# Kernel tuning notes

Hardware: AMD Instinct MI355X
Metric: run time of the kernel (lower is better)

The kernel has to match this reference:

```python
import jax, jax.numpy as jnp
import numpy as np

BATCH = 64
ORIGINAL_DIM = 524288
PROJ_DIM = 8192
C = 4


def setup_inputs() -> dict:
    key = jax.random.key(0)
    k1, k2, k3 = jax.random.split(key, 3)
    x = jax.random.normal(k1, (BATCH, ORIGINAL_DIM), dtype=jnp.float32)
    rand_indices = jax.random.randint(k2, (ORIGINAL_DIM, C), 0, PROJ_DIM, dtype=jnp.int32)
    rand_signs = jax.random.randint(k3, (ORIGINAL_DIM, C), 0, 2, dtype=jnp.int32)
    return {"x": x, "rand_indices": rand_indices, "rand_signs": rand_signs}


def reference(x, rand_indices, rand_signs):
    # SJLT: out[b, rand_indices[d, j]] += x[b, d] * sign[d, j], scaled by 1/sqrt(c)
    B, D = x.shape
    c = rand_indices.shape[1]
    signs = (2 * rand_signs - 1).astype(x.dtype)  # {0,1} -> {-1,+1}
    scale = 1.0 / jnp.sqrt(jnp.asarray(c, dtype=x.dtype))
    out = jnp.zeros((B, PROJ_DIM), dtype=x.dtype)
    for j in range(c):  # small fixed loop over non-zeros per column
        out = out.at[:, rand_indices[:, j]].add(x * signs[:, j])
    return out * scale
```

## Files before the change

### kernel.cpp

```cpp
#include <hip/hip_runtime.h>


constexpr int BATCH = 64;
constexpr int DIM   = 524288;
constexpr int PROJ  = 8192;
constexpr int NENT  = DIM * 4;
constexpr int NBLKA = 256;
constexpr int EPB   = NENT / NBLKA;
constexpr int NHB   = 512;
constexpr int HBP   = PROJ / NHB;
constexpr int CAPH  = 4608;
constexpr int TBLK  = 2048;

__device__ __forceinline__ uint32_t f2bf(float f) {
    uint32_t u = __float_as_uint(f);
    return (u + 0x7fffu + ((u >> 16) & 1u)) >> 16;
}

__global__ __launch_bounds__(1024) void prep_kernel(
    const float* __restrict__ x, const int4* __restrict__ idx4,
    const int4* __restrict__ sgn4, uint32_t* __restrict__ gBase,
    uint32_t* __restrict__ dense, uint32_t* __restrict__ xT)
{
    __shared__ uint32_t sh[10260];
    const int t = threadIdx.x;

    if (blockIdx.x < NBLKA) {
        uint32_t* cntL    = sh;
        uint32_t* offL    = sh + 512;
        uint32_t* curL    = sh + 1024;
        uint32_t* wsum    = sh + 1536;
        uint32_t* gb      = sh + 1544;
        uint32_t* staging = sh + 2056;
        const int lane = t & 63;
        const int blk  = blockIdx.x;

        if (t < NHB) cntL[t] = 0;
        __syncthreads();

        int4 iv[2], sv[2];
        int  dd[2];
#pragma unroll
        for (int j = 0; j < 2; ++j) {
            int d = blk * 2048 + j * 1024 + t;
            dd[j] = d;
            iv[j] = idx4[d];
            sv[j] = sgn4[d];
        }
#pragma unroll
        for (int j = 0; j < 2; ++j) {
            atomicAdd(&cntL[(uint32_t)iv[j].x >> 4], 1u);
            atomicAdd(&cntL[(uint32_t)iv[j].y >> 4], 1u);
            atomicAdd(&cntL[(uint32_t)iv[j].z >> 4], 1u);
            atomicAdd(&cntL[(uint32_t)iv[j].w >> 4], 1u);
        }
        __syncthreads();
        uint32_t v = 0, s = 0;
        if (t < NHB) {
            s = cntL[t]; v = s;
#pragma unroll
            for (int off = 1; off < 64; off <<= 1) {
                uint32_t u = __shfl_up(v, off);
                if (lane >= off) v += u;
            }
            if (lane == 63) wsum[t >> 6] = v;
        }
        __syncthreads();
        if (t < NHB) {
            uint32_t wb = 0;
            for (int w0 = 0; w0 < (t >> 6); ++w0) wb += wsum[w0];
            uint32_t ex = wb + v - s;
            offL[t] = ex;
            curL[t] = ex;
        }
        __syncthreads();
#pragma unroll
        for (int j = 0; j < 2; ++j) {
            const uint32_t dv = (uint32_t)dd[j] << 1;
            int p, ss;
            uint32_t b, sl;
            p = iv[j].x; ss = sv[j].x & 1; b = (uint32_t)p >> 4;
            sl = atomicAdd(&curL[b], 1u);
            staging[sl] = ((uint32_t)(p & 15) << 20) | dv | (uint32_t)ss;
            p = iv[j].y; ss = sv[j].y & 1; b = (uint32_t)p >> 4;
            sl = atomicAdd(&curL[b], 1u);
            staging[sl] = ((uint32_t)(p & 15) << 20) | dv | (uint32_t)ss;
            p = iv[j].z; ss = sv[j].z & 1; b = (uint32_t)p >> 4;
            sl = atomicAdd(&curL[b], 1u);
            staging[sl] = ((uint32_t)(p & 15) << 20) | dv | (uint32_t)ss;
            p = iv[j].w; ss = sv[j].w & 1; b = (uint32_t)p >> 4;
            sl = atomicAdd(&curL[b], 1u);
            staging[sl] = ((uint32_t)(p & 15) << 20) | dv | (uint32_t)ss;
        }
        __syncthreads();
        if (t < NHB) gb[t] = atomicAdd(&gBase[t], cntL[t]);
        __syncthreads();
        const int w = t >> 6;
        for (int i = 0; i < NHB / 16; ++i) {
            const int b = w * (NHB / 16) + i;
            const uint32_t c   = cntL[b];
            const uint32_t src = offL[b];
            const uint32_t g0  = gb[b];
            const uint32_t lim = (g0 < (uint32_t)CAPH) ? ((uint32_t)CAPH - g0) : 0u;
            const uint32_t cw  = c < lim ? c : lim;
            uint32_t* dst = dense + (size_t)b * CAPH + g0;
            for (uint32_t j2 = lane; j2 < cw; j2 += 64) dst[j2] = staging[src + j2];
        }
    } else {
        float* tile = reinterpret_cast<float*>(sh);
        const int blk   = blockIdx.x - NBLKA;
        const int dbase = blk * 256;
        const int c  = t & 15;
        const int r  = t >> 4;
        const int a  = t & 15;
        const int dr = t >> 4;
#pragma unroll
        for (int it = 0; it < 4; ++it) {
            const int d0 = dbase + it * 64;
            float4 v = *reinterpret_cast<const float4*>(
                &x[(size_t)r * DIM + d0 + 4 * c]);
            __syncthreads();
            tile[r * 65 + 4 * c + 0] = v.x;
            tile[r * 65 + 4 * c + 1] = v.y;
            tile[r * 65 + 4 * c + 2] = v.z;
            tile[r * 65 + 4 * c + 3] = v.w;
            __syncthreads();
            uint32_t lo, hi;
            lo = f2bf(tile[(4 * a + 0) * 65 + dr] * 0.5f);
            hi = f2bf(tile[(4 * a + 1) * 65 + dr] * 0.5f);
            const uint32_t w0 = lo | (hi << 16);
            lo = f2bf(tile[(4 * a + 2) * 65 + dr] * 0.5f);
            hi = f2bf(tile[(4 * a + 3) * 65 + dr] * 0.5f);
            const uint32_t w1 = lo | (hi << 16);
            uint2 wv; wv.x = w0; wv.y = w1;
            *reinterpret_cast<uint2*>(&xT[(size_t)(d0 + dr) * 32 + 2 * a]) = wv;
        }
    }
}

#define G9_CASE(Q) case Q: acc0[Q] += v0; acc1[Q] += v1; break;
#define G9_SWITCH(PV)                                                     \
    switch (PV) {                                                         \
        G9_CASE(0)  G9_CASE(1)  G9_CASE(2)  G9_CASE(3)                    \
        G9_CASE(4)  G9_CASE(5)  G9_CASE(6)  G9_CASE(7)                    \
        G9_CASE(8)  G9_CASE(9)  G9_CASE(10) G9_CASE(11)                   \
        G9_CASE(12) G9_CASE(13) G9_CASE(14) G9_CASE(15)                   \
        default: break;                                                   \
    }

__global__ __launch_bounds__(1024) void gather9_kernel(
    const uint32_t* __restrict__ dense, const uint32_t* __restrict__ gBase,
    const uint32_t* __restrict__ xT, float* __restrict__ out)
{
    __shared__ float2 red2[8 * 528];
    const int t    = threadIdx.x;
    const int w    = t >> 6;
    const int lane = t & 63;
    const int k    = lane & 31;
    const int hb   = blockIdx.x;

    uint32_t nt = gBase[hb];
    if (nt > (uint32_t)CAPH) nt = (uint32_t)CAPH;
    const uint32_t* seg = dense + (size_t)hb * CAPH;
    const uint32_t s0 = (nt * (uint32_t)w) >> 4;
    const uint32_t s1 = (nt * (uint32_t)(w + 1)) >> 4;

    float acc0[16], acc1[16];
#pragma unroll
    for (int q = 0; q < 16; ++q) { acc0[q] = 0.f; acc1[q] = 0.f; }

    uint32_t base = s0;
    for (; base + 8 <= s1; base += 8) {
        uint32_t e8[8];
#pragma unroll
        for (int j = 0; j < 8; ++j) e8[j] = seg[base + j];
        uint32_t u8[8];
#pragma unroll
        for (int j = 0; j < 8; ++j)
            u8[j] = xT[(size_t)((e8[j] >> 1) & 0x7FFFFu) * 32 + k];
#pragma unroll
        for (int j = 0; j < 8; ++j) {
            const uint32_t u = u8[j] ^ ((e8[j] & 1u) ? 0u : 0x80008000u);
            const float v0 = __uint_as_float(u << 16);
            const float v1 = __uint_as_float(u & 0xffff0000u);
            const int pv = __builtin_amdgcn_readfirstlane((int)((e8[j] >> 20) & 15u));
            G9_SWITCH(pv)
        }
    }
    for (; base < s1; ++base) {
        const uint32_t e = seg[base];
        uint32_t u = xT[(size_t)((e >> 1) & 0x7FFFFu) * 32 + k];
        u ^= (e & 1u) ? 0u : 0x80008000u;
        const float v0 = __uint_as_float(u << 16);
        const float v1 = __uint_as_float(u & 0xffff0000u);
        const int pv = __builtin_amdgcn_readfirstlane((int)((e >> 20) & 15u));
        G9_SWITCH(pv)
    }

#pragma unroll
    for (int stride = 8; stride >= 1; stride >>= 1) {
        if (w >= stride && w < 2 * stride && lane < 32) {
            float2* dst = red2 + (w - stride) * 528;
#pragma unroll
            for (int q = 0; q < 16; ++q)
                dst[q * 33 + k] = make_float2(acc0[q], acc1[q]);
        }
        __syncthreads();
        if (w < stride && lane < 32) {
            const float2* src = red2 + w * 528;
#pragma unroll
            for (int q = 0; q < 16; ++q) {
                float2 v = src[q * 33 + k];
                acc0[q] += v.x; acc1[q] += v.y;
            }
        }
        __syncthreads();
    }
    if (w == 0 && lane < 32) {
#pragma unroll
        for (int q = 0; q < 16; ++q)
            red2[q * 33 + k] = make_float2(acc0[q], acc1[q]);
    }
    __syncthreads();
    {
        const int b = t >> 4, q = t & 15;
        const float2 vq = red2[q * 33 + (b >> 1)];
        out[(size_t)b * PROJ + hb * HBP + q] = (b & 1) ? vq.y : vq.x;
    }
}

__device__ __forceinline__ void lds_fadd(uint32_t byte_addr, float v) {
    asm volatile("ds_add_f32 %0, %1" :: "v"(byte_addr), "v"(v) : "memory");
}
__device__ __forceinline__ void lds_fadd_off32k(uint32_t byte_addr, float v) {
    asm volatile("ds_add_f32 %0, %1 offset:32768" :: "v"(byte_addr), "v"(v) : "memory");
}

__global__ __launch_bounds__(1024) void sjlt_scatter(
    const float* __restrict__ x, const int4* __restrict__ idx4,
    const int4* __restrict__ sgn4, float* __restrict__ out)
{
    __shared__ float acc[4 * PROJ];
    for (int i = threadIdx.x; i < 4 * PROJ; i += 1024) acc[i] = 0.0f;
    __syncthreads();
    const int row0 = blockIdx.y * 4;
    const int dbeg = blockIdx.x * (DIM / 16);
    const uint32_t accBase = (uint32_t)(uintptr_t)(&acc[0]);
    const float* xr0 = x + (size_t)(row0 + 0) * DIM;
    const float* xr1 = x + (size_t)(row0 + 1) * DIM;
    const float* xr2 = x + (size_t)(row0 + 2) * DIM;
    const float* xr3 = x + (size_t)(row0 + 3) * DIM;
    for (int d = dbeg + (int)threadIdx.x; d < dbeg + DIM / 16; d += 1024) {
        const int4 iv = idx4[d];
        const int4 sv = sgn4[d];
        const uint32_t u0 = __float_as_uint(xr0[d]);
        const uint32_t u1 = __float_as_uint(xr1[d]);
        const uint32_t u2 = __float_as_uint(xr2[d]);
        const uint32_t u3 = __float_as_uint(xr3[d]);
        const int p[4] = {iv.x, iv.y, iv.z, iv.w};
        const int s[4] = {sv.x, sv.y, sv.z, sv.w};
#pragma unroll
        for (int j = 0; j < 4; ++j) {
            const uint32_t flip = (uint32_t)(s[j] ^ 1) << 31;
            const uint32_t a01  = accBase + ((uint32_t)p[j] << 2);
            const uint32_t a23  = a01 + 2u * 32768u;
            lds_fadd        (a01, __uint_as_float(u0 ^ flip));
            lds_fadd_off32k (a01, __uint_as_float(u1 ^ flip));
            lds_fadd        (a23, __uint_as_float(u2 ^ flip));
            lds_fadd_off32k (a23, __uint_as_float(u3 ^ flip));
        }
    }
    __syncthreads();
    for (int i = threadIdx.x; i < 4 * PROJ; i += 1024) {
        const int r  = i >> 13;
        const int pp = i & (PROJ - 1);
        unsafeAtomicAdd(&out[(size_t)(row0 + r) * PROJ + pp], acc[i] * 0.5f);
    }
}

extern "C" void kernel_launch(void* const* d_in, const int* in_sizes, int n_in,
                              void* d_out, int out_size, void* d_ws, size_t ws_size,
                              hipStream_t stream) {
    const float* x   = (const float*)d_in[0];
    const int4*  idx = (const int4*) d_in[1];
    const int4*  sgn = (const int4*) d_in[2];
    float*       out = (float*)d_out;

    const size_t need = ((size_t)NHB + (size_t)NHB * CAPH + (size_t)DIM * 32) * 4;

    if (ws_size >= need) {
        uint32_t* gBase = (uint32_t*)d_ws;
        uint32_t* dense = gBase + NHB;
        uint32_t* xT    = dense + (size_t)NHB * CAPH;

        hipMemsetAsync(gBase, 0, NHB * sizeof(uint32_t), stream);
        prep_kernel   <<<NBLKA + TBLK, 1024, 0, stream>>>(
            x, idx, sgn, gBase, dense, xT);
        gather9_kernel<<<NHB,          1024, 0, stream>>>(dense, gBase, xT, out);
    } else {
        hipMemsetAsync(d_out, 0, (size_t)out_size * sizeof(float), stream);
        dim3 grid(16, 16);
        sjlt_scatter<<<grid, 1024, 0, stream>>>(x, idx, sgn, out);
    }
}
```

Measured before the change: 295.9 us.

## Replace count-scan bucketing with fixed-capacity LDS slots and global overflow

The bucketing phase drops the per-block histogram count, prefix scan and extra barriers. It now gives each of the 512 hash buckets a fixed 28-entry LDS slot and sends overflow entries straight to global memory through a global atomic. Blocks are halved in size (1024 columns each, doubling the block count), and the flush loop assigns 8 lanes per bucket instead of a full wave. This removes a pass of LDS atomics and syncs per block, at the cost of more global atomics on overflow, a larger shared array, and more blocks each paying a global atomicAdd on gBase.

```diff
diff --git a/kernel.cpp b/kernel.cpp
--- a/kernel.cpp
+++ b/kernel.cpp
@@ -5,8 +5,8 @@
 constexpr int DIM   = 524288;
 constexpr int PROJ  = 8192;
 constexpr int NENT  = DIM * 4;
-constexpr int NBLKA = 256;
-constexpr int EPB   = NENT / NBLKA;
+constexpr int NBLKA = 512;
+constexpr int SCAP  = 28;
 constexpr int NHB   = 512;
 constexpr int HBP   = PROJ / NHB;
 constexpr int CAPH  = 4608;
@@ -22,89 +22,69 @@
     const int4* __restrict__ sgn4, uint32_t* __restrict__ gBase,
     uint32_t* __restrict__ dense, uint32_t* __restrict__ xT)
 {
-    __shared__ uint32_t sh[10260];
+    __shared__ uint32_t sh[15360];
     const int t = threadIdx.x;
 
     if (blockIdx.x < NBLKA) {
-        uint32_t* cntL    = sh;
-        uint32_t* offL    = sh + 512;
-        uint32_t* curL    = sh + 1024;
-        uint32_t* wsum    = sh + 1536;
-        uint32_t* gb      = sh + 1544;
-        uint32_t* staging = sh + 2056;
+        uint32_t* curL    = sh;
+        uint32_t* gb      = sh + 512;
+        uint32_t* staging = sh + 1024;
         const int lane = t & 63;
         const int blk  = blockIdx.x;
 
-        if (t < NHB) cntL[t] = 0;
-        __syncthreads();
-
-        int4 iv[2], sv[2];
-        int  dd[2];
-#pragma unroll
-        for (int j = 0; j < 2; ++j) {
-            int d = blk * 2048 + j * 1024 + t;
-            dd[j] = d;
-            iv[j] = idx4[d];
-            sv[j] = sgn4[d];
-        }
-#pragma unroll
-        for (int j = 0; j < 2; ++j) {
-            atomicAdd(&cntL[(uint32_t)iv[j].x >> 4], 1u);
-            atomicAdd(&cntL[(uint32_t)iv[j].y >> 4], 1u);
-            atomicAdd(&cntL[(uint32_t)iv[j].z >> 4], 1u);
-            atomicAdd(&cntL[(uint32_t)iv[j].w >> 4], 1u);
-        }
-        __syncthreads();
-        uint32_t v = 0, s = 0;
+        if (t < NHB) curL[t] = (uint32_t)t * SCAP;
+        __syncthreads();
+
+        const int d  = blk * 1024 + t;
+        const int4 iv = idx4[d];
+        const int4 sv = sgn4[d];
+        const uint32_t dv = (uint32_t)d << 1;
+        {
+            uint32_t b, sl, pay;
+            b = (uint32_t)iv.x >> 4;
+            pay = (((uint32_t)iv.x & 15u) << 20) | dv | (uint32_t)(sv.x & 1);
+            sl = atomicAdd(&curL[b], 1u);
+            if (sl < (b + 1u) * SCAP) staging[sl] = pay;
+            else { uint32_t g = atomicAdd(&gBase[b], 1u);
+                   if (g < (uint32_t)CAPH) dense[(size_t)b * CAPH + g] = pay; }
+            b = (uint32_t)iv.y >> 4;
+            pay = (((uint32_t)iv.y & 15u) << 20) | dv | (uint32_t)(sv.y & 1);
+            sl = atomicAdd(&curL[b], 1u);
+            if (sl < (b + 1u) * SCAP) staging[sl] = pay;
+            else { uint32_t g = atomicAdd(&gBase[b], 1u);
+                   if (g < (uint32_t)CAPH) dense[(size_t)b * CAPH + g] = pay; }
+            b = (uint32_t)iv.z >> 4;
+            pay = (((uint32_t)iv.z & 15u) << 20) | dv | (uint32_t)(sv.z & 1);
+            sl = atomicAdd(&curL[b], 1u);
+            if (sl < (b + 1u) * SCAP) staging[sl] = pay;
+            else { uint32_t g = atomicAdd(&gBase[b], 1u);
+                   if (g < (uint32_t)CAPH) dense[(size_t)b * CAPH + g] = pay; }
+            b = (uint32_t)iv.w >> 4;
+            pay = (((uint32_t)iv.w & 15u) << 20) | dv | (uint32_t)(sv.w & 1);
+            sl = atomicAdd(&curL[b], 1u);
+            if (sl < (b + 1u) * SCAP) staging[sl] = pay;
+            else { uint32_t g = atomicAdd(&gBase[b], 1u);
+                   if (g < (uint32_t)CAPH) dense[(size_t)b * CAPH + g] = pay; }
+        }
+        __syncthreads();
         if (t < NHB) {
-            s = cntL[t]; v = s;
-#pragma unroll
-            for (int off = 1; off < 64; off <<= 1) {
-                uint32_t u = __shfl_up(v, off);
-                if (lane >= off) v += u;
-            }
-            if (lane == 63) wsum[t >> 6] = v;
-        }
-        __syncthreads();
-        if (t < NHB) {
-            uint32_t wb = 0;
-            for (int w0 = 0; w0 < (t >> 6); ++w0) wb += wsum[w0];
-            uint32_t ex = wb + v - s;
-            offL[t] = ex;
-            curL[t] = ex;
-        }
-        __syncthreads();
-#pragma unroll
-        for (int j = 0; j < 2; ++j) {
-            const uint32_t dv = (uint32_t)dd[j] << 1;
-            int p, ss;
-            uint32_t b, sl;
-            p = iv[j].x; ss = sv[j].x & 1; b = (uint32_t)p >> 4;
-            sl = atomicAdd(&curL[b], 1u);
-            staging[sl] = ((uint32_t)(p & 15) << 20) | dv | (uint32_t)ss;
-            p = iv[j].y; ss = sv[j].y & 1; b = (uint32_t)p >> 4;
-            sl = atomicAdd(&curL[b], 1u);
-            staging[sl] = ((uint32_t)(p & 15) << 20) | dv | (uint32_t)ss;
-            p = iv[j].z; ss = sv[j].z & 1; b = (uint32_t)p >> 4;
-            sl = atomicAdd(&curL[b], 1u);
-            staging[sl] = ((uint32_t)(p & 15) << 20) | dv | (uint32_t)ss;
-            p = iv[j].w; ss = sv[j].w & 1; b = (uint32_t)p >> 4;
-            sl = atomicAdd(&curL[b], 1u);
-            staging[sl] = ((uint32_t)(p & 15) << 20) | dv | (uint32_t)ss;
-        }
-        __syncthreads();
-        if (t < NHB) gb[t] = atomicAdd(&gBase[t], cntL[t]);
+            uint32_t cnt = curL[t] - (uint32_t)t * SCAP;
+            if (cnt > (uint32_t)SCAP) cnt = (uint32_t)SCAP;
+            curL[t] = cnt;
+            gb[t]   = atomicAdd(&gBase[t], cnt);
+        }
         __syncthreads();
         const int w = t >> 6;
-        for (int i = 0; i < NHB / 16; ++i) {
-            const int b = w * (NHB / 16) + i;
-            const uint32_t c   = cntL[b];
-            const uint32_t src = offL[b];
-            const uint32_t g0  = gb[b];
+        const int g = lane >> 3, li = lane & 7;
+        for (int r = 0; r < 4; ++r) {
+            const int hb = w * 32 + r * 8 + g;
+            const uint32_t cnt = curL[hb];
+            const uint32_t g0  = gb[hb];
             const uint32_t lim = (g0 < (uint32_t)CAPH) ? ((uint32_t)CAPH - g0) : 0u;
-            const uint32_t cw  = c < lim ? c : lim;
-            uint32_t* dst = dense + (size_t)b * CAPH + g0;
-            for (uint32_t j2 = lane; j2 < cw; j2 += 64) dst[j2] = staging[src + j2];
+            const uint32_t cw  = cnt < lim ? cnt : lim;
+            uint32_t* dst = dense + (size_t)hb * CAPH + g0;
+            const uint32_t* src2 = staging + hb * SCAP;
+            for (uint32_t j2 = li; j2 < cw; j2 += 8) dst[j2] = src2[j2];
         }
     } else {
         float* tile = reinterpret_cast<float*>(sh);
```

Result: no change. 300.3 us (+1.5%).
